# Kernel optimization log

Hardware: AMD Instinct MI355X
Metric: run time of the kernel (lower is better)

The kernel has to match this reference:

```python
import jax, jax.numpy as jnp
import numpy as np

B, S, HID = 2, 2048, 1024
NH, NKV, HD = 16, 8, 128
EPS = 1e-6
THETA = 1.0e6
NEG = -1e9

def _rope_tables():
    inv_freq = 1.0 / (THETA ** (np.arange(0, HD, 2, dtype=np.float32) / HD))  # [HD/2]
    pos = np.arange(S, dtype=np.float32)
    freqs = np.outer(pos, inv_freq)                      # [S, HD/2]
    emb = np.concatenate([freqs, freqs], axis=-1)        # [S, HD]
    cos = np.broadcast_to(np.cos(emb), (B, S, HD)).copy()
    sin = np.broadcast_to(np.sin(emb), (B, S, HD)).copy()
    return jnp.asarray(cos), jnp.asarray(sin)

def setup_inputs() -> dict:
    key = jax.random.key(0)
    ks = jax.random.split(key, 8)
    hidden_states = jax.random.normal(ks[0], (B, S, HID), jnp.float32)
    cos, sin = _rope_tables()
    # additive causal mask [B,1,S,S]
    causal = jnp.triu(jnp.full((S, S), NEG, jnp.float32), k=1)
    attention_mask = jnp.broadcast_to(causal[None, None], (B, 1, S, S))
    std = 0.02
    Wq = jax.random.normal(ks[1], (NH * HD, HID), jnp.float32) * std
    Wk = jax.random.normal(ks[2], (NKV * HD, HID), jnp.float32) * std
    Wv = jax.random.normal(ks[3], (NKV * HD, HID), jnp.float32) * std
    Wo = jax.random.normal(ks[4], (HID, NH * HD), jnp.float32) * std
    q_norm_w = jnp.ones((HD,), jnp.float32)
    k_norm_w = jnp.ones((HD,), jnp.float32)
    return {"hidden_states": hidden_states, "cos": cos, "sin": sin,
            "attention_mask": attention_mask, "Wq": Wq, "Wk": Wk, "Wv": Wv,
            "Wo": Wo, "q_norm_w": q_norm_w, "k_norm_w": k_norm_w}

def _rms_norm(x, w):
    var = jnp.mean(jnp.square(x), axis=-1, keepdims=True)
    return x * jax.lax.rsqrt(var + EPS) * w

def _rotate_half(x):
    x1, x2 = jnp.split(x, 2, axis=-1)
    return jnp.concatenate([-x2, x1], axis=-1)

def reference(hidden_states, cos, sin, attention_mask, Wq, Wk, Wv, Wo, q_norm_w, k_norm_w):
    # projections: [B,S,heads,HD] -> [B,heads,S,HD]
    q = jnp.einsum('bsh,dh->bsd', hidden_states, Wq).reshape(B, S, NH, HD)
    k = jnp.einsum('bsh,dh->bsd', hidden_states, Wk).reshape(B, S, NKV, HD)
    v = jnp.einsum('bsh,dh->bsd', hidden_states, Wv).reshape(B, S, NKV, HD)
    q = jnp.transpose(_rms_norm(q, q_norm_w), (0, 2, 1, 3))
    k = jnp.transpose(_rms_norm(k, k_norm_w), (0, 2, 1, 3))
    v = jnp.transpose(v, (0, 2, 1, 3))
    c = cos[:, None]  # [B,1,S,HD]
    s = sin[:, None]
    q = q * c + _rotate_half(q) * s
    k = k * c + _rotate_half(k) * s
    # repeat kv heads: NKV -> NH
    n_rep = NH // NKV
    k = jnp.repeat(k, n_rep, axis=1)
    v = jnp.repeat(v, n_rep, axis=1)
    scaling = HD ** -0.5
    scores = jnp.einsum('bhqd,bhkd->bhqk', q, k) * scaling
    scores = scores + attention_mask
    probs = jax.nn.softmax(scores.astype(jnp.float32), axis=-1).astype(q.dtype)
    out = jnp.einsum('bhqk,bhkd->bhqd', probs, v)
    out = jnp.transpose(out, (0, 2, 1, 3)).reshape(B, S, NH * HD)
    return jnp.einsum('bsd,hd->bsh', out, Wo)
```

## Files before the change

kernel.cpp:

```cpp
#include <hip/hip_runtime.h>
#include <hip/hip_fp16.h>


typedef _Float16 f16;
typedef __attribute__((ext_vector_type(8))) _Float16 f16x8;
typedef __attribute__((ext_vector_type(4))) _Float16 f16x4;
typedef __attribute__((ext_vector_type(4))) float f32x4;

__constant__ const float kEps = 1e-6f;
__constant__ const float kScaleL2 = 0.1275179120685481f;

#define ASYNC_LD16(gp, lp)                                              \
  __builtin_amdgcn_global_load_lds(                                     \
      (const __attribute__((address_space(1))) void*)(gp),              \
      (__attribute__((address_space(3))) void*)(uint32_t)(uintptr_t)(lp), 16, 0, 0)

__global__ __launch_bounds__(256) void cast_all(
    const float* __restrict__ h, const float* __restrict__ wq,
    const float* __restrict__ wk, const float* __restrict__ wv,
    const float* __restrict__ wo, f16* __restrict__ hb,
    f16* __restrict__ wqkv, f16* __restrict__ wob) {
  const int idx = blockIdx.x * 256 + threadIdx.x;
  const float* src;
  f16* dst;
  int base;
  if (idx < 1048576) { src = h;  dst = hb;                  base = 0; }
  else if (idx < 1572864) { src = wq; dst = wqkv;               base = 1048576; }
  else if (idx < 1835008) { src = wk; dst = wqkv + 2048 * 1024; base = 1572864; }
  else if (idx < 2097152) { src = wv; dst = wqkv + 3072 * 1024; base = 1835008; }
  else { src = wo; dst = wob; base = 2097152; }
  const int i = (idx - base) * 4;
  f32x4 v = *reinterpret_cast<const f32x4*>(src + i);
  f16x4 o;
  o.x = (f16)v.x; o.y = (f16)v.y; o.z = (f16)v.z; o.w = (f16)v.w;
  *reinterpret_cast<f16x4*>(dst + i) = o;
}

__global__ __launch_bounds__(256) void gemm_bt_h(const f16* __restrict__ A,
                                                 const f16* __restrict__ Bm,
                                                 f16* __restrict__ C,
                                                 int M, int N, int K) {
  __shared__ __align__(16) f16 As[128][64];
  __shared__ __align__(16) f16 Bs[128][64];
  const int tid = threadIdx.x;
  const int lane = tid & 63;
  const int wave = tid >> 6;
  const int cl = lane & 15;
  const int quad = lane >> 4;
  const int wm = (wave >> 1) * 64;
  const int wn = (wave & 1) * 64;
  const int tm = blockIdx.y * 128;
  const int tn = blockIdx.x * 128;
  const int r0 = tid >> 3;
  const int csw = ((tid & 7) ^ (r0 & 7)) * 8;

  const f16* Ab = A + (size_t)(tm + r0) * K + csw;
  const f16* Bb = Bm + (size_t)(tn + r0) * K + csw;
  char* Al = (char*)As + wave * 1024;
  char* Bl = (char*)Bs + wave * 1024;

  f32x4 acc[4][4] = {};

  for (int k0 = 0; k0 < K; k0 += 64) {
#pragma unroll
    for (int c = 0; c < 4; ++c) {
      ASYNC_LD16(Ab + (size_t)(c * 32) * K + k0, Al + c * 4096);
      ASYNC_LD16(Bb + (size_t)(c * 32) * K + k0, Bl + c * 4096);
    }
    __syncthreads();
#pragma unroll
    for (int kk = 0; kk < 2; ++kk) {
      f16x8 af[4], bf[4];
#pragma unroll
      for (int mi = 0; mi < 4; ++mi)
        af[mi] = *reinterpret_cast<const f16x8*>(
            &As[wm + mi * 16 + cl][((kk * 4 + quad) ^ (cl & 7)) * 8]);
#pragma unroll
      for (int ni = 0; ni < 4; ++ni)
        bf[ni] = *reinterpret_cast<const f16x8*>(
            &Bs[wn + ni * 16 + cl][((kk * 4 + quad) ^ (cl & 7)) * 8]);
#pragma unroll
      for (int mi = 0; mi < 4; ++mi)
#pragma unroll
        for (int ni = 0; ni < 4; ++ni)
          acc[mi][ni] =
              __builtin_amdgcn_mfma_f32_16x16x32_f16(af[mi], bf[ni], acc[mi][ni], 0, 0, 0);
    }
    __syncthreads();
  }
#pragma unroll
  for (int mi = 0; mi < 4; ++mi)
#pragma unroll
    for (int ni = 0; ni < 4; ++ni)
#pragma unroll
      for (int r = 0; r < 4; ++r)
        C[(size_t)(tm + wm + mi * 16 + quad * 4 + r) * N + tn + wn + ni * 16 + cl] =
            (f16)acc[mi][ni][r];
}

__global__ __launch_bounds__(256) void gemm_bt64(const f16* __restrict__ A,
                                                 const f16* __restrict__ Bm,
                                                 float* __restrict__ C,
                                                 int M, int N, int K) {
  __shared__ __align__(16) f16 As[64][64];
  __shared__ __align__(16) f16 Bs[128][64];
  const int tid = threadIdx.x;
  const int lane = tid & 63;
  const int wave = tid >> 6;
  const int cl = lane & 15;
  const int quad = lane >> 4;
  const int wm = (wave >> 1) * 32;
  const int wn = (wave & 1) * 64;
  const int tm = blockIdx.y * 64;
  const int tn = blockIdx.x * 128;
  const int r0 = tid >> 3;
  const int csw = ((tid & 7) ^ (r0 & 7)) * 8;

  const f16* Ab = A + (size_t)(tm + r0) * K + csw;
  const f16* Bb = Bm + (size_t)(tn + r0) * K + csw;
  char* Al = (char*)As + wave * 1024;
  char* Bl = (char*)Bs + wave * 1024;

  f32x4 acc[2][4] = {};

  for (int k0 = 0; k0 < K; k0 += 64) {
#pragma unroll
    for (int c = 0; c < 2; ++c)
      ASYNC_LD16(Ab + (size_t)(c * 32) * K + k0, Al + c * 4096);
#pragma unroll
    for (int c = 0; c < 4; ++c)
      ASYNC_LD16(Bb + (size_t)(c * 32) * K + k0, Bl + c * 4096);
    __syncthreads();
#pragma unroll
    for (int kk = 0; kk < 2; ++kk) {
      f16x8 af[2], bf[4];
#pragma unroll
      for (int mi = 0; mi < 2; ++mi)
        af[mi] = *reinterpret_cast<const f16x8*>(
            &As[wm + mi * 16 + cl][((kk * 4 + quad) ^ (cl & 7)) * 8]);
#pragma unroll
      for (int ni = 0; ni < 4; ++ni)
        bf[ni] = *reinterpret_cast<const f16x8*>(
            &Bs[wn + ni * 16 + cl][((kk * 4 + quad) ^ (cl & 7)) * 8]);
#pragma unroll
      for (int mi = 0; mi < 2; ++mi)
#pragma unroll
        for (int ni = 0; ni < 4; ++ni)
          acc[mi][ni] =
              __builtin_amdgcn_mfma_f32_16x16x32_f16(af[mi], bf[ni], acc[mi][ni], 0, 0, 0);
    }
    __syncthreads();
  }
#pragma unroll
  for (int mi = 0; mi < 2; ++mi)
#pragma unroll
    for (int ni = 0; ni < 4; ++ni)
#pragma unroll
      for (int r = 0; r < 4; ++r)
        C[(size_t)(tm + wm + mi * 16 + quad * 4 + r) * N + tn + wn + ni * 16 + cl] =
            acc[mi][ni][r];
}

__global__ __launch_bounds__(256) void rope_norm(
    const f16* __restrict__ qkvh,
    const float* __restrict__ cosT, const float* __restrict__ sinT,
    const float* __restrict__ qw, const float* __restrict__ kw,
    f16* __restrict__ qt, f16* __restrict__ kt) {
  const int gw = blockIdx.x * 4 + (threadIdx.x >> 6);
  const int lane = threadIdx.x & 63;
  const int head = gw % 24;
  const int bs = gw / 24;
  const bool isq = head < 16;
  const f16* src = qkvh + (size_t)bs * 4096 +
                   (isq ? head * 128 : 2048 + (head - 16) * 128);
  const float x1 = (float)src[lane];
  const float x2 = (float)src[lane + 64];
  float ss = x1 * x1 + x2 * x2;
#pragma unroll
  for (int off = 32; off >= 1; off >>= 1) ss += __shfl_xor(ss, off);
  const float rms = rsqrtf(ss * (1.0f / 128.0f) + kEps);
  const float* w = isq ? qw : kw;
  const float n1 = x1 * rms * w[lane];
  const float n2 = x2 * rms * w[lane + 64];
  const float* cb = cosT + (size_t)bs * 128;
  const float* sb = sinT + (size_t)bs * 128;
  const float o1 = n1 * cb[lane] - n2 * sb[lane];
  const float o2 = n2 * cb[lane + 64] + n1 * sb[lane + 64];
  const int b = bs >> 11;
  const int s = bs & 2047;
  f16* dst;
  float sc;
  if (isq) {
    dst = qt + ((size_t)(b * 16 + head) * 2048 + s) * 128;
    sc = kScaleL2;
  } else {
    dst = kt + ((size_t)(b * 8 + (head - 16)) * 2048 + s) * 128;
    sc = 1.0f;
  }
  dst[lane] = (f16)(o1 * sc);
  dst[lane + 64] = (f16)(o2 * sc);
}

__global__ __launch_bounds__(256) void v_transpose(const f16* __restrict__ qkvh,
                                                   f16* __restrict__ vt) {
  __shared__ __align__(16) f16 tile[64][136];
  const int bh = blockIdx.y;
  const int b = bh >> 3, h = bh & 7;
  const int s0 = blockIdx.x * 64;
  const int tid = threadIdx.x;
#pragma unroll
  for (int i = 0; i < 4; ++i) {
    int c = tid + i * 256;
    int s = c >> 4;
    int cg = c & 15;
    f16x8 v = *reinterpret_cast<const f16x8*>(
        qkvh + (size_t)(b * 2048 + s0 + s) * 4096 + 3072 + h * 128 + cg * 8);
    *reinterpret_cast<f16x8*>(&tile[s][cg * 8]) = v;
  }
  __syncthreads();
#pragma unroll
  for (int i = 0; i < 4; ++i) {
    int c = tid + i * 256;
    int d = c >> 3;
    int sB = (c & 7) * 8;
    f16x8 o;
#pragma unroll
    for (int j = 0; j < 8; ++j) o[j] = tile[sB + j][d];
    *reinterpret_cast<f16x8*>(vt + ((size_t)(b * 8 + h) * 128 + d) * 2048 + s0 + sB) = o;
  }
}

__global__ __launch_bounds__(128) void attn(const f16* __restrict__ Qt,
                                            const f16* __restrict__ Kt,
                                            const f16* __restrict__ Vt,
                                            f16* __restrict__ Ot) {
  __shared__ __align__(16) f16 Ks[64 * 128];
  __shared__ __align__(16) f16 Vs[128 * 64];
  __shared__ __align__(16) f16 Ps[2][32][72];

  const int bid = blockIdx.x;
  const int bh = bid & 31;
  const int t = 31 - (bid >> 5);
  const int q0 = t * 64;
  const int b = bh >> 4, h = bh & 15;
  const int kv = h >> 1;

  const int tid = threadIdx.x;
  const int lane = tid & 63, wv = tid >> 6;
  const int cl = lane & 15, quad = lane >> 4;
  const int qw0 = q0 + wv * 32;

  const f16* qbase = Qt + ((size_t)(b * 16 + h) * 2048 + qw0 + cl) * 128;
  f16x8 aq[2][4];
#pragma unroll
  for (int mi = 0; mi < 2; ++mi)
#pragma unroll
    for (int kk = 0; kk < 4; ++kk)
      aq[mi][kk] =
          *reinterpret_cast<const f16x8*>(qbase + mi * 16 * 128 + kk * 32 + quad * 8);

  const f16* kbase = Kt + (size_t)(b * 8 + kv) * 2048 * 128;
  const f16* vbase = Vt + (size_t)(b * 8 + kv) * 128 * 2048;

  float m_[2] = {-1e30f, -1e30f}, l_[2] = {0.f, 0.f};
  f32x4 oacc[2][8] = {};

  for (int kt0 = 0; kt0 <= q0; kt0 += 64) {
#pragma unroll
    for (int i = 0; i < 8; ++i) {
      const int c = (wv * 8 + i) * 64 + lane;
      const int kr = c >> 4, kg = c & 15;
      const int kgs = (kg & 8) | ((kg & 7) ^ (kr & 7));
      ASYNC_LD16(kbase + (size_t)(kt0 + kr) * 128 + kgs * 8,
                 (char*)Ks + (wv * 8 + i) * 1024);
      const int vr = c >> 3, vg = c & 7;
      const int vgs = vg ^ (vr & 7);
      ASYNC_LD16(vbase + (size_t)vr * 2048 + kt0 + vgs * 8,
                 (char*)Vs + (wv * 8 + i) * 1024);
    }
    __syncthreads();
    f32x4 sacc[2][4] = {};
#pragma unroll
    for (int kk = 0; kk < 4; ++kk)
#pragma unroll
      for (int ni = 0; ni < 4; ++ni) {
        const int gk = kk * 4 + quad;
        const int gks = (gk & 8) | ((gk & 7) ^ (cl & 7));
        f16x8 ak =
            *reinterpret_cast<const f16x8*>(Ks + (ni * 16 + cl) * 128 + gks * 8);
#pragma unroll
        for (int mi = 0; mi < 2; ++mi)
          sacc[mi][ni] =
              __builtin_amdgcn_mfma_f32_16x16x32_f16(ak, aq[mi][kk], sacc[mi][ni], 0, 0, 0);
      }
    if (kt0 == q0) {
#pragma unroll
      for (int mi = 0; mi < 2; ++mi) {
        const int qg = qw0 + mi * 16 + cl;
#pragma unroll
        for (int ni = 0; ni < 4; ++ni) {
          const int sg = kt0 + ni * 16 + quad * 4;
#pragma unroll
          for (int r = 0; r < 4; ++r)
            if (sg + r > qg) sacc[mi][ni][r] = -1e30f;
        }
      }
    }
    float al[2];
#pragma unroll
    for (int mi = 0; mi < 2; ++mi) {
      float m0 = sacc[mi][0][0];
#pragma unroll
      for (int ni = 0; ni < 4; ++ni)
#pragma unroll
        for (int r = 0; r < 4; ++r) m0 = fmaxf(m0, sacc[mi][ni][r]);
      m0 = fmaxf(m0, __shfl_xor(m0, 16));
      m0 = fmaxf(m0, __shfl_xor(m0, 32));
      const float nm = fmaxf(m_[mi], m0);
      al[mi] = __builtin_amdgcn_exp2f(m_[mi] - nm);
      m_[mi] = nm;
      float ps = 0.f;
#pragma unroll
      for (int ni = 0; ni < 4; ++ni)
#pragma unroll
        for (int r = 0; r < 4; ++r) {
          const float p = __builtin_amdgcn_exp2f(sacc[mi][ni][r] - nm);
          sacc[mi][ni][r] = p;
          ps += p;
        }
      l_[mi] = l_[mi] * al[mi] + ps;
    }
#pragma unroll
    for (int mi = 0; mi < 2; ++mi)
#pragma unroll
      for (int ni = 0; ni < 4; ++ni) {
        f16x4 pk;
#pragma unroll
        for (int r = 0; r < 4; ++r) pk[r] = (f16)sacc[mi][ni][r];
        *reinterpret_cast<f16x4*>(&Ps[wv][mi * 16 + cl][ni * 16 + quad * 4]) = pk;
      }
#pragma unroll
    for (int mi = 0; mi < 2; ++mi)
#pragma unroll
      for (int dg = 0; dg < 8; ++dg) oacc[mi][dg] *= al[mi];
    asm volatile("s_waitcnt lgkmcnt(0)" ::: "memory");
    f16x8 bp[2][2];
#pragma unroll
    for (int mi = 0; mi < 2; ++mi)
#pragma unroll
      for (int kh = 0; kh < 2; ++kh)
        bp[mi][kh] =
            *reinterpret_cast<const f16x8*>(&Ps[wv][mi * 16 + cl][kh * 32 + quad * 8]);
#pragma unroll
    for (int kh = 0; kh < 2; ++kh)
#pragma unroll
      for (int dg = 0; dg < 8; ++dg) {
        const int gv = kh * 4 + quad;
        const int gvs = gv ^ (cl & 7);
        f16x8 av =
            *reinterpret_cast<const f16x8*>(Vs + (dg * 16 + cl) * 64 + gvs * 8);
#pragma unroll
        for (int mi = 0; mi < 2; ++mi)
          oacc[mi][dg] =
              __builtin_amdgcn_mfma_f32_16x16x32_f16(av, bp[mi][kh], oacc[mi][dg], 0, 0, 0);
      }
    __syncthreads();
  }
#pragma unroll
  for (int mi = 0; mi < 2; ++mi) {
    float l = l_[mi];
    l += __shfl_xor(l, 16);
    l += __shfl_xor(l, 32);
    const float inv = 1.0f / l;
    const size_t qg = qw0 + mi * 16 + cl;
#pragma unroll
    for (int dg = 0; dg < 8; ++dg) {
      f16x4 o;
#pragma unroll
      for (int r = 0; r < 4; ++r) o[r] = (f16)(oacc[mi][dg][r] * inv);
      *reinterpret_cast<f16x4*>(Ot + ((size_t)b * 2048 + qg) * 2048 + h * 128 +
                                dg * 16 + quad * 4) = o;
    }
  }
}

extern "C" void kernel_launch(void* const* d_in, const int* in_sizes, int n_in,
                              void* d_out, int out_size, void* d_ws, size_t ws_size,
                              hipStream_t stream) {
  (void)in_sizes; (void)n_in; (void)out_size; (void)ws_size;
  const float* hidden = (const float*)d_in[0];
  const float* cosT = (const float*)d_in[1];
  const float* sinT = (const float*)d_in[2];
  const float* Wq = (const float*)d_in[4];
  const float* Wk = (const float*)d_in[5];
  const float* Wv = (const float*)d_in[6];
  const float* Wo = (const float*)d_in[7];
  const float* qnw = (const float*)d_in[8];
  const float* knw = (const float*)d_in[9];
  float* out = (float*)d_out;

  char* ws = (char*)d_ws;
  size_t off = 0;
  auto alloc = [&](size_t bytes) {
    char* p = ws + off;
    off += (bytes + 255) & ~(size_t)255;
    return p;
  };
  f16* hb = (f16*)alloc(4096ull * 1024 * 2);
  f16* wqkv = (f16*)alloc(4096ull * 1024 * 2);
  f16* wob = (f16*)alloc(1024ull * 2048 * 2);
  f16* qkvh = (f16*)alloc(4096ull * 4096 * 2);
  f16* qt = (f16*)alloc(32ull * 2048 * 128 * 2);
  f16* kt = (f16*)alloc(16ull * 2048 * 128 * 2);
  f16* vt = (f16*)alloc(16ull * 2048 * 128 * 2);
  f16* ot = (f16*)alloc(4096ull * 2048 * 2);

  cast_all<<<10240, 256, 0, stream>>>(hidden, Wq, Wk, Wv, Wo, hb, wqkv, wob);

  gemm_bt_h<<<dim3(32, 32), 256, 0, stream>>>(hb, wqkv, qkvh, 4096, 4096, 1024);

  rope_norm<<<24576, 256, 0, stream>>>(qkvh, cosT, sinT, qnw, knw, qt, kt);
  v_transpose<<<dim3(32, 16), 256, 0, stream>>>(qkvh, vt);

  attn<<<1024, 128, 0, stream>>>(qt, kt, vt, ot);

  gemm_bt64<<<dim3(8, 64), 256, 0, stream>>>(ot, wob, out, 4096, 1024, 2048);
}
```

Baseline: 304.0 us.

## Fuse RMSNorm, RoPE and V transpose into the QKV GEMM epilogue

The QKV projection GEMM now performs per-head RMS normalization (reduced with DPP and shared memory), applies rotary embedding, and writes Q/K directly in head-major layout. V tiles are written transposed straight from the accumulators. This removes the intermediate qkvh buffer round trip and two extra kernel launches. In exchange the epilogue gets heavier, with shared-memory staging, an extra barrier and strided transposed V stores.

```diff
diff --git a/kernel.cpp b/kernel.cpp
--- a/kernel.cpp
+++ b/kernel.cpp
@@ -14,6 +14,19 @@
   __builtin_amdgcn_global_load_lds(                                     \
       (const __attribute__((address_space(1))) void*)(gp),              \
       (__attribute__((address_space(3))) void*)(uint32_t)(uintptr_t)(lp), 16, 0, 0)
+
+__device__ __forceinline__ float dpp_sum16(float v) {
+  int x;
+  x = __builtin_amdgcn_update_dpp(0, __builtin_bit_cast(int, v), 0xB1, 0xF, 0xF, true);
+  v += __builtin_bit_cast(float, x);
+  x = __builtin_amdgcn_update_dpp(0, __builtin_bit_cast(int, v), 0x4E, 0xF, 0xF, true);
+  v += __builtin_bit_cast(float, x);
+  x = __builtin_amdgcn_update_dpp(0, __builtin_bit_cast(int, v), 0x141, 0xF, 0xF, true);
+  v += __builtin_bit_cast(float, x);
+  x = __builtin_amdgcn_update_dpp(0, __builtin_bit_cast(int, v), 0x140, 0xF, 0xF, true);
+  v += __builtin_bit_cast(float, x);
+  return v;
+}
 
 __global__ __launch_bounds__(256) void cast_all(
     const float* __restrict__ h, const float* __restrict__ wq,
@@ -36,12 +49,18 @@
   *reinterpret_cast<f16x4*>(dst + i) = o;
 }
 
-__global__ __launch_bounds__(256) void gemm_bt_h(const f16* __restrict__ A,
-                                                 const f16* __restrict__ Bm,
-                                                 f16* __restrict__ C,
-                                                 int M, int N, int K) {
-  __shared__ __align__(16) f16 As[128][64];
-  __shared__ __align__(16) f16 Bs[128][64];
+__global__ __launch_bounds__(256) void gemm_qkv(
+    const f16* __restrict__ A, const f16* __restrict__ Bm,
+    const float* __restrict__ qnw, const float* __restrict__ knw,
+    const float* __restrict__ cosT, const float* __restrict__ sinT,
+    f16* __restrict__ qt, f16* __restrict__ kt, f16* __restrict__ vt) {
+  __shared__ __align__(16) char smem[35840];
+  f16 (*As)[64] = reinterpret_cast<f16(*)[64]>(smem);
+  f16 (*Bs)[64] = reinterpret_cast<f16(*)[64]>(smem + 16384);
+  f16 (*Ct)[136] = reinterpret_cast<f16(*)[136]>(smem);
+  float* rsq = reinterpret_cast<float*>(smem + 34816);
+
+  const int K = 1024, tn = blockIdx.x, tm = blockIdx.y;
   const int tid = threadIdx.x;
   const int lane = tid & 63;
   const int wave = tid >> 6;
@@ -49,15 +68,13 @@
   const int quad = lane >> 4;
   const int wm = (wave >> 1) * 64;
   const int wn = (wave & 1) * 64;
-  const int tm = blockIdx.y * 128;
-  const int tn = blockIdx.x * 128;
   const int r0 = tid >> 3;
   const int csw = ((tid & 7) ^ (r0 & 7)) * 8;
 
-  const f16* Ab = A + (size_t)(tm + r0) * K + csw;
-  const f16* Bb = Bm + (size_t)(tn + r0) * K + csw;
-  char* Al = (char*)As + wave * 1024;
-  char* Bl = (char*)Bs + wave * 1024;
+  const f16* Ab = A + (size_t)(tm * 128 + r0) * K + csw;
+  const f16* Bb = Bm + (size_t)(tn * 128 + r0) * K + csw;
+  char* Al = smem + wave * 1024;
+  char* Bl = smem + 16384 + wave * 1024;
 
   f32x4 acc[4][4] = {};
 
@@ -88,14 +105,84 @@
     }
     __syncthreads();
   }
+
+  const int b = tm >> 4;
+  const int s0 = (tm & 15) * 128;
+
+  if (tn >= 24) {
+    const int h = tn - 24;
+    f16* vbase = vt + (size_t)(b * 8 + h) * 128 * 2048;
+#pragma unroll
+    for (int mi = 0; mi < 4; ++mi) {
+      const int sg = s0 + wm + mi * 16 + quad * 4;
+#pragma unroll
+      for (int ni = 0; ni < 4; ++ni) {
+        const int d = wn + ni * 16 + cl;
+        f16x4 o;
+#pragma unroll
+        for (int r = 0; r < 4; ++r) o[r] = (f16)acc[mi][ni][r];
+        *reinterpret_cast<f16x4*>(vbase + (size_t)d * 2048 + sg) = o;
+      }
+    }
+    return;
+  }
+
+  float s2[4][4];
 #pragma unroll
   for (int mi = 0; mi < 4; ++mi)
 #pragma unroll
-    for (int ni = 0; ni < 4; ++ni)
+    for (int r = 0; r < 4; ++r) {
+      float v = 0.f;
+#pragma unroll
+      for (int ni = 0; ni < 4; ++ni) v += acc[mi][ni][r] * acc[mi][ni][r];
+      s2[mi][r] = dpp_sum16(v);
+    }
+#pragma unroll
+  for (int mi = 0; mi < 4; ++mi) {
+    const int srow = wm + mi * 16 + quad * 4;
+    if (cl == 0) {
 #pragma unroll
       for (int r = 0; r < 4; ++r)
-        C[(size_t)(tm + wm + mi * 16 + quad * 4 + r) * N + tn + wn + ni * 16 + cl] =
-            (f16)acc[mi][ni][r];
+        rsq[(wave & 1) * 128 + srow + r] = s2[mi][r];
+    }
+#pragma unroll
+    for (int ni = 0; ni < 4; ++ni) {
+      const int d = wn + ni * 16 + cl;
+#pragma unroll
+      for (int r = 0; r < 4; ++r) Ct[srow + r][d] = (f16)acc[mi][ni][r];
+    }
+  }
+  __syncthreads();
+
+  const bool isq = tn < 16;
+  const int h = isq ? tn : tn - 16;
+  const float* wv_ = isq ? qnw : knw;
+  const float osc = isq ? kScaleL2 : 1.0f;
+  f16* obase = isq ? qt + (size_t)(b * 16 + h) * 2048 * 128
+                   : kt + (size_t)(b * 8 + h) * 2048 * 128;
+#pragma unroll
+  for (int i = 0; i < 8; ++i) {
+    const int idx = tid + i * 256;
+    const int srow = idx >> 4;
+    const int d0 = (idx & 15) * 8;
+    const int dp = d0 ^ 64;
+    const float sgn = (d0 < 64) ? -1.f : 1.f;
+    const float rq = rsq[srow] + rsq[128 + srow];
+    const float rms = rsqrtf(rq * (1.0f / 128.0f) + kEps);
+    const int grow = tm * 128 + srow;
+    const float* cb = cosT + (size_t)grow * 128;
+    const float* sb = sinT + (size_t)grow * 128;
+    f16x8 x = *reinterpret_cast<const f16x8*>(&Ct[srow][d0]);
+    f16x8 xp = *reinterpret_cast<const f16x8*>(&Ct[srow][dp]);
+    f16x8 o;
+#pragma unroll
+    for (int j = 0; j < 8; ++j) {
+      const float n = (float)x[j] * rms * wv_[d0 + j];
+      const float np = (float)xp[j] * rms * wv_[dp + j];
+      o[j] = (f16)((n * cb[d0 + j] + sgn * np * sb[d0 + j]) * osc);
+    }
+    *reinterpret_cast<f16x8*>(obase + (size_t)(s0 + srow) * 128 + d0) = o;
+  }
 }
 
 __global__ __launch_bounds__(256) void gemm_bt64(const f16* __restrict__ A,
@@ -161,75 +248,6 @@
             acc[mi][ni][r];
 }
 
-__global__ __launch_bounds__(256) void rope_norm(
-    const f16* __restrict__ qkvh,
-    const float* __restrict__ cosT, const float* __restrict__ sinT,
-    const float* __restrict__ qw, const float* __restrict__ kw,
-    f16* __restrict__ qt, f16* __restrict__ kt) {
-  const int gw = blockIdx.x * 4 + (threadIdx.x >> 6);
-  const int lane = threadIdx.x & 63;
-  const int head = gw % 24;
-  const int bs = gw / 24;
-  const bool isq = head < 16;
-  const f16* src = qkvh + (size_t)bs * 4096 +
-                   (isq ? head * 128 : 2048 + (head - 16) * 128);
-  const float x1 = (float)src[lane];
-  const float x2 = (float)src[lane + 64];
-  float ss = x1 * x1 + x2 * x2;
-#pragma unroll
-  for (int off = 32; off >= 1; off >>= 1) ss += __shfl_xor(ss, off);
-  const float rms = rsqrtf(ss * (1.0f / 128.0f) + kEps);
-  const float* w = isq ? qw : kw;
-  const float n1 = x1 * rms * w[lane];
-  const float n2 = x2 * rms * w[lane + 64];
-  const float* cb = cosT + (size_t)bs * 128;
-  const float* sb = sinT + (size_t)bs * 128;
-  const float o1 = n1 * cb[lane] - n2 * sb[lane];
-  const float o2 = n2 * cb[lane + 64] + n1 * sb[lane + 64];
-  const int b = bs >> 11;
-  const int s = bs & 2047;
-  f16* dst;
-  float sc;
-  if (isq) {
-    dst = qt + ((size_t)(b * 16 + head) * 2048 + s) * 128;
-    sc = kScaleL2;
-  } else {
-    dst = kt + ((size_t)(b * 8 + (head - 16)) * 2048 + s) * 128;
-    sc = 1.0f;
-  }
-  dst[lane] = (f16)(o1 * sc);
-  dst[lane + 64] = (f16)(o2 * sc);
-}
-
-__global__ __launch_bounds__(256) void v_transpose(const f16* __restrict__ qkvh,
-                                                   f16* __restrict__ vt) {
-  __shared__ __align__(16) f16 tile[64][136];
-  const int bh = blockIdx.y;
-  const int b = bh >> 3, h = bh & 7;
-  const int s0 = blockIdx.x * 64;
-  const int tid = threadIdx.x;
-#pragma unroll
-  for (int i = 0; i < 4; ++i) {
-    int c = tid + i * 256;
-    int s = c >> 4;
-    int cg = c & 15;
-    f16x8 v = *reinterpret_cast<const f16x8*>(
-        qkvh + (size_t)(b * 2048 + s0 + s) * 4096 + 3072 + h * 128 + cg * 8);
-    *reinterpret_cast<f16x8*>(&tile[s][cg * 8]) = v;
-  }
-  __syncthreads();
-#pragma unroll
-  for (int i = 0; i < 4; ++i) {
-    int c = tid + i * 256;
-    int d = c >> 3;
-    int sB = (c & 7) * 8;
-    f16x8 o;
-#pragma unroll
-    for (int j = 0; j < 8; ++j) o[j] = tile[sB + j][d];
-    *reinterpret_cast<f16x8*>(vt + ((size_t)(b * 8 + h) * 128 + d) * 2048 + s0 + sB) = o;
-  }
-}
-
 __global__ __launch_bounds__(128) void attn(const f16* __restrict__ Qt,
                                             const f16* __restrict__ Kt,
                                             const f16* __restrict__ Vt,
@@ -409,7 +427,6 @@
   f16* hb = (f16*)alloc(4096ull * 1024 * 2);
   f16* wqkv = (f16*)alloc(4096ull * 1024 * 2);
   f16* wob = (f16*)alloc(1024ull * 2048 * 2);
-  f16* qkvh = (f16*)alloc(4096ull * 4096 * 2);
   f16* qt = (f16*)alloc(32ull * 2048 * 128 * 2);
   f16* kt = (f16*)alloc(16ull * 2048 * 128 * 2);
   f16* vt = (f16*)alloc(16ull * 2048 * 128 * 2);
@@ -417,10 +434,8 @@
 
   cast_all<<<10240, 256, 0, stream>>>(hidden, Wq, Wk, Wv, Wo, hb, wqkv, wob);
 
-  gemm_bt_h<<<dim3(32, 32), 256, 0, stream>>>(hb, wqkv, qkvh, 4096, 4096, 1024);
-
-  rope_norm<<<24576, 256, 0, stream>>>(qkvh, cosT, sinT, qnw, knw, qt, kt);
-  v_transpose<<<dim3(32, 16), 256, 0, stream>>>(qkvh, vt);
+  gemm_qkv<<<dim3(32, 32), 256, 0, stream>>>(hb, wqkv, qnw, knw, cosT, sinT,
+                                             qt, kt, vt);
 
   attn<<<1024, 128, 0, stream>>>(qt, kt, vt, ot);
 
```

Measured after the change: 311.5 us. 2.5% more time.
